# Performance work log

Measured on AMD Instinct MI355X. Metric: run time of the kernel, lower is better.

The kernel has to match this reference:

```python
import jax, jax.numpy as jnp
import numpy as np

D_MODEL = 1024
N_HEADS = 16
HEAD_DIM = D_MODEL // N_HEADS
MAX_REL = 16
SEQ = 1024
BATCH = 4


def _rel_embed(table, length_q, length_k):
    # table: [2*MAX_REL+1, head_dim] -> [lq, lk, head_dim]
    dist = jnp.arange(length_k)[None, :] - jnp.arange(length_q)[:, None]
    idx = jnp.clip(dist, -MAX_REL, MAX_REL) + MAX_REL
    return table[idx]


def setup_inputs() -> dict:
    key = jax.random.key(0)
    ks = jax.random.split(key, 16)
    s = 1.0 / np.sqrt(D_MODEL)
    inp = {
        "query": jax.random.normal(ks[0], (BATCH, SEQ, D_MODEL), jnp.float32),
        "key": jax.random.normal(ks[1], (BATCH, SEQ, D_MODEL), jnp.float32),
        "value": jax.random.normal(ks[2], (BATCH, SEQ, D_MODEL), jnp.float32),
        "mask": jnp.ones((BATCH, SEQ, SEQ), jnp.int32),
        "Wq": jax.random.normal(ks[3], (D_MODEL, D_MODEL), jnp.float32) * s,
        "bq": jnp.zeros((D_MODEL,), jnp.float32),
        "Wk": jax.random.normal(ks[4], (D_MODEL, D_MODEL), jnp.float32) * s,
        "bk": jnp.zeros((D_MODEL,), jnp.float32),
        "Wv": jax.random.normal(ks[5], (D_MODEL, D_MODEL), jnp.float32) * s,
        "bv": jnp.zeros((D_MODEL,), jnp.float32),
        "Wo": jax.random.normal(ks[6], (D_MODEL, D_MODEL), jnp.float32) * s,
        "bo": jnp.zeros((D_MODEL,), jnp.float32),
        "emb_k": jax.random.normal(ks[7], (2 * MAX_REL + 1, HEAD_DIM), jnp.float32) * 0.1,
        "emb_v": jax.random.normal(ks[8], (2 * MAX_REL + 1, HEAD_DIM), jnp.float32) * 0.1,
    }
    return inp


def reference(query, key, value, mask, Wq, bq, Wk, bk, Wv, bv, Wo, bo, emb_k, emb_v):
    B, lq, _ = query.shape
    H, hd = N_HEADS, HEAD_DIM
    scale = jnp.sqrt(jnp.asarray(hd, query.dtype))

    q = (query @ Wq.T + bq).reshape(B, lq, H, hd)   # [B,S,H,hd]
    k = (key @ Wk.T + bk).reshape(B, lq, H, hd)
    v = (value @ Wv.T + bv).reshape(B, lq, H, hd)

    # content-content term
    attn1 = jnp.einsum("bqhd,bkhd->bhqk", q, k)
    # content-position term: r_k2[q,k,d]
    r_k2 = _rel_embed(emb_k, lq, lq)               # [S,S,hd]
    attn2 = jnp.einsum("bqhd,qkd->bhqk", q, r_k2)

    attn = (attn1 + attn2) / scale
    attn = jnp.where(mask[:, None, :, :] == 0, -jnp.inf, attn)
    attn = jax.nn.softmax(attn, axis=-1)           # [B,H,S,S]

    weight1 = jnp.einsum("bhqk,bkhd->bhqd", attn, v)
    r_v2 = _rel_embed(emb_v, lq, lq)               # [S,S,hd]
    weight2 = jnp.einsum("bhqk,qkd->bhqd", attn, r_v2)

    x = (weight1 + weight2).transpose(0, 2, 1, 3).reshape(B, lq, H * hd)
    return x @ Wo.T + bo
```

## Files before the change

### kernel.cpp

```cpp
#include <hip/hip_runtime.h>
#include <math.h>

#define D_MODEL 1024
#define N_HEADS 16
#define HEAD_DIM 64
#define MAX_REL 16
#define SEQ 1024
#define BATCH 4

typedef _Float16 f16x8 __attribute__((ext_vector_type(8)));
typedef _Float16 f16x4 __attribute__((ext_vector_type(4)));
typedef _Float16 f16x2 __attribute__((ext_vector_type(2)));
typedef float f32x4 __attribute__((ext_vector_type(4)));
typedef unsigned long long u64;

__device__ __forceinline__ void gld_lds16(const _Float16* g, _Float16* l) {
    __builtin_amdgcn_global_load_lds(
        (const __attribute__((address_space(1))) void*)(uintptr_t)g,
        (__attribute__((address_space(3))) void*)(uintptr_t)l, 16, 0, 0);
}

__global__ __launch_bounds__(256) void mask_compress(
    const int* __restrict__ mask, u64* __restrict__ mbits, int n64)
{
    const int wid  = (blockIdx.x * 256 + threadIdx.x) >> 6;
    const int lane = threadIdx.x & 63;
    if (wid < n64) {
        const int vv = mask[(size_t)wid * 64 + lane];
        const u64 bal = __ballot(vv != 0);
        if (lane == 0) mbits[wid] = bal;
    }
}

__global__ __launch_bounds__(256) void cvt_all(
    const float* __restrict__ q, const float* __restrict__ k, const float* __restrict__ v,
    const float* __restrict__ Wq, const float* __restrict__ Wk,
    const float* __restrict__ Wv, const float* __restrict__ Wo,
    _Float16* __restrict__ qin, _Float16* __restrict__ kin, _Float16* __restrict__ vin,
    _Float16* __restrict__ wq, _Float16* __restrict__ wk,
    _Float16* __restrict__ wv, _Float16* __restrict__ wo)
{
    const size_t M1 = 1u << 20;
    size_t f = ((size_t)blockIdx.x * 256 + threadIdx.x) * 4;
    const float* src; _Float16* dst; size_t off;
    if (f < 4*M1)       { src = q; dst = qin; off = f; }
    else if (f < 8*M1)  { src = k; dst = kin; off = f - 4*M1; }
    else if (f < 12*M1) { src = v; dst = vin; off = f - 8*M1; }
    else {
        int u = (int)(f >> 20) - 12;
        src = (u==0)?Wq:(u==1)?Wk:(u==2)?Wv:Wo;
        dst = (u==0)?wq:(u==1)?wk:(u==2)?wv:wo;
        off = f & (M1 - 1);
    }
    float4 x = *(const float4*)(src + off);
    f16x4 h; h[0]=(_Float16)x.x; h[1]=(_Float16)x.y; h[2]=(_Float16)x.z; h[3]=(_Float16)x.w;
    *(f16x4*)(dst + off) = h;
}

#define TBM 64
#define TBN 64
#define TBK 64

template <typename CT>
__global__ __launch_bounds__(256, 4) void gemm_f16async(
    const _Float16* A0, const _Float16* A1, const _Float16* A2,
    const _Float16* W0, const _Float16* W1, const _Float16* W2,
    const float* b0, const float* b1, const float* b2,
    CT* C0, CT* C1, CT* C2, int M, int N, int K)
{
    __shared__ _Float16 As[2][TBM * TBK];
    __shared__ _Float16 Ws[2][TBN * TBK];

    const int z = blockIdx.z;
    const _Float16* A = (z==0)?A0:(z==1)?A1:A2;
    const _Float16* W = (z==0)?W0:(z==1)?W1:W2;
    const float* bias = (z==0)?b0:(z==1)?b1:b2;
    CT* C = (z==0)?C0:(z==1)?C1:C2;

    const int tid = threadIdx.x;
    const int lane = tid & 63;
    const int w = tid >> 6;
    const int quad = lane >> 4;
    const int l16 = lane & 15;
    const int m0 = blockIdx.y * TBM;
    const int n0 = blockIdx.x * TBN;
    const int wm = (w & 1) * 32;
    const int wn = (w >> 1) * 32;

    int em[2], ek[2];
    #pragma unroll
    for (int i = 0; i < 2; ++i) {
        const int e = i * 256 + tid;
        em[i] = e >> 3;
        ek[i] = (e & 7) ^ (em[i] & 7);
    }

    f32x4 acc[2][2];
    #pragma unroll
    for (int i = 0; i < 2; ++i)
        #pragma unroll
        for (int j = 0; j < 2; ++j)
            acc[i][j] = (f32x4){0.f, 0.f, 0.f, 0.f};

    const int nk = K / TBK;

    #pragma unroll
    for (int i = 0; i < 2; ++i) {
        const int e = i * 256 + tid;
        gld_lds16(A + (size_t)(m0 + em[i]) * K + ek[i] * 8, &As[0][e * 8]);
        gld_lds16(W + (size_t)(n0 + em[i]) * K + ek[i] * 8, &Ws[0][e * 8]);
    }
    __syncthreads();

    for (int it = 0; it < nk; ++it) {
        const int cur = it & 1, nb = cur ^ 1;

        if (it + 1 < nk) {
            const int kt = (it + 1) * TBK;
            #pragma unroll
            for (int i = 0; i < 2; ++i) {
                const int e = i * 256 + tid;
                gld_lds16(A + (size_t)(m0 + em[i]) * K + kt + ek[i] * 8, &As[nb][e * 8]);
                gld_lds16(W + (size_t)(n0 + em[i]) * K + kt + ek[i] * 8, &Ws[nb][e * 8]);
            }
        }

        #pragma unroll
        for (int ks = 0; ks < 2; ++ks) {
            const int k8 = ks * 4 + quad;
            f16x8 af[2], bf[2];
            #pragma unroll
            for (int i = 0; i < 2; ++i) {
                const int m = wm + i * 16 + l16;
                af[i] = *(const f16x8*)&As[cur][m * 64 + ((k8 ^ (m & 7)) * 8)];
            }
            #pragma unroll
            for (int j = 0; j < 2; ++j) {
                const int n = wn + j * 16 + l16;
                bf[j] = *(const f16x8*)&Ws[cur][n * 64 + ((k8 ^ (n & 7)) * 8)];
            }
            #pragma unroll
            for (int i = 0; i < 2; ++i)
                #pragma unroll
                for (int j = 0; j < 2; ++j)
                    acc[i][j] = __builtin_amdgcn_mfma_f32_16x16x32_f16(af[i], bf[j], acc[i][j], 0, 0, 0);
        }
        __syncthreads();
    }

    const int cbase = n0 + wn + l16;
    const int rbase = m0 + wm + quad * 4;
    #pragma unroll
    for (int j = 0; j < 2; ++j) {
        const int col = cbase + j * 16;
        const float bv = bias[col];
        #pragma unroll
        for (int i = 0; i < 2; ++i) {
            #pragma unroll
            for (int r = 0; r < 4; ++r) {
                const int m = rbase + i * 16 + r;
                C[(size_t)m * N + col] = (CT)(acc[i][j][r] + bv);
            }
        }
    }
}

#define QT 64
#define KT 64
#define SP 72
#define EVW 32
#define NT (SEQ/KT)

__global__ __launch_bounds__(256, 2) void attn_flash_mfma3(
    const _Float16* __restrict__ q, const _Float16* __restrict__ kg,
    const _Float16* __restrict__ v, const u64* __restrict__ mbits,
    const float* __restrict__ emb_k, const float* __restrict__ emb_v,
    _Float16* __restrict__ x)
{
    __shared__ _Float16 Ks[2][KT * HEAD_DIM];
    __shared__ _Float16 Vt[2][HEAD_DIM * SP];
    __shared__ _Float16 Ps[QT * SP];
    __shared__ _Float16 EvT[HEAD_DIM * EVW];
    __shared__ _Float16 pbh[QT * 33];
    __shared__ _Float16 bandh[QT * 33];

    const int qt = blockIdx.x, h = blockIdx.y, b = blockIdx.z;
    const int q0 = qt * QT;
    const int tid = threadIdx.x;
    const int lane = tid & 63;
    const int w = tid >> 6;
    const int quad = lane >> 4;
    const int l16 = lane & 15;
    const int qrow = w * 16 + quad * 4;

    const int vk = (tid & 31) * 2, vd = (tid >> 5) * 8;
    const int k8 = vk >> 3, klo = vk & 7;
    const int sr = tid >> 2, sc = (tid & 3) * 16;

    const float CS = 0.18033688011112042f;
    const float M8 = 8.0f;

    #pragma unroll
    for (int i = 0; i < 2; ++i) {
        const int e = i * 256 + tid;
        const int row = e >> 3;
        const int k8s = (e & 7) ^ (row & 7);
        gld_lds16(kg + ((size_t)(b*SEQ + row))*D_MODEL + h*HEAD_DIM + k8s*8, &Ks[0][e*8]);
    }

    f16x8 qf[2];
    {
        const _Float16* qp = q + ((size_t)(b*SEQ + q0 + w*16 + l16))*D_MODEL + h*HEAD_DIM;
        qf[0] = *(const f16x8*)(qp + quad*8);
        qf[1] = *(const f16x8*)(qp + 32 + quad*8);
    }

    f16x8 vp0, vp1;
    {
        const _Float16* vp = v + ((size_t)(b*SEQ + vk))*D_MODEL + h*HEAD_DIM + vd;
        vp0 = *(const f16x8*)(vp);
        vp1 = *(const f16x8*)(vp + D_MODEL);
    }

    if (sr < 48) {
        #pragma unroll
        for (int c = 0; c < 16; ++c) {
            float val = (sr < 33) ? emb_k[sr*HEAD_DIM + sc + c] : 0.f;
            Ps[sr*SP + sc + c] = (_Float16)val;
        }
    }
    for (int idx = tid; idx < HEAD_DIM*EVW; idx += 256) {
        const int d = idx >> 5, j = idx & 31;
        EvT[d*EVW + j] = (_Float16)emb_v[j*HEAD_DIM + d];
    }
    for (int i = tid; i < QT*33; i += 256) bandh[i] = (_Float16)(-60000.f);
    __syncthreads();

    {
        f32x4 accP[3];
        #pragma unroll
        for (int jt = 0; jt < 3; ++jt) accP[jt] = (f32x4){0.f,0.f,0.f,0.f};
        #pragma unroll
        for (int ks2 = 0; ks2 < 2; ++ks2) {
            const int ko = ks2*32 + quad*8;
            #pragma unroll
            for (int jt = 0; jt < 3; ++jt) {
                f16x8 bf = *(const f16x8*)&Ps[(jt*16 + l16)*SP + ko];
                accP[jt] = __builtin_amdgcn_mfma_f32_16x16x32_f16(qf[ks2], bf, accP[jt], 0, 0, 0);
            }
        }
        #pragma unroll
        for (int jt = 0; jt < 3; ++jt) {
            const int j = jt*16 + l16;
            if (j < 33) {
                #pragma unroll
                for (int r = 0; r < 4; ++r) pbh[(qrow + r)*33 + j] = (_Float16)(accP[jt][r] * CS);
            }
        }
    }
    __syncthreads();

    #pragma unroll
    for (int i = 0; i < 8; ++i) {
        const int d = vd + i;
        const int xd = (d >> 3) & 7;
        f16x2 pr; pr[0] = vp0[i]; pr[1] = vp1[i];
        *(f16x2*)&Vt[0][d*SP + ((k8 ^ xd) << 3) + klo] = pr;
    }
    __syncthreads();

    f32x4 accO[4];
    #pragma unroll
    for (int dt = 0; dt < 4; ++dt) accO[dt] = (f32x4){0.f,0.f,0.f,0.f};
    f32x4 accL = (f32x4){0.f,0.f,0.f,0.f};
    f32x4 accRT = (f32x4){0.f,0.f,0.f,0.f};
    float rt1[4] = {0.f,0.f,0.f,0.f};

    f16x8 ones;
    #pragma unroll
    for (int i = 0; i < 8; ++i) ones[i] = (_Float16)1.0f;

    const int kxl = l16 & 7;

    for (int t = 0; t < NT; ++t) {
        const int cur = t & 1, nb = cur ^ 1;
        const int k0 = t * KT;
        const int kq = k0 - q0;
        const int mode = (kq <= -128) ? 0 : (kq >= 128 ? 2 : 1);

        if (t + 1 < NT) {
            #pragma unroll
            for (int i = 0; i < 2; ++i) {
                const int e = i * 256 + tid;
                const int row = e >> 3;
                const int k8s = (e & 7) ^ (row & 7);
                gld_lds16(kg + ((size_t)(b*SEQ + k0 + KT + row))*D_MODEL + h*HEAD_DIM + k8s*8, &Ks[nb][e*8]);
            }
            const _Float16* vp = v + ((size_t)(b*SEQ + k0 + KT + vk))*D_MODEL + h*HEAD_DIM + vd;
            vp0 = *(const f16x8*)(vp);
            vp1 = *(const f16x8*)(vp + D_MODEL);
        }

        u64 mw[4];
        {
            const u64* mb = mbits + ((size_t)(b*SEQ + q0 + qrow)) * (SEQ/64) + t;
            #pragma unroll
            for (int r = 0; r < 4; ++r) mw[r] = mb[(size_t)r * (SEQ/64)];
        }

        f32x4 accS[4];
        #pragma unroll
        for (int jt = 0; jt < 4; ++jt) accS[jt] = (f32x4){0.f,0.f,0.f,0.f};
        #pragma unroll
        for (int ks2 = 0; ks2 < 2; ++ks2) {
            const int slot = (ks2*4 + quad) ^ kxl;
            #pragma unroll
            for (int jt = 0; jt < 4; ++jt) {
                f16x8 bf = *(const f16x8*)&Ks[cur][(jt*16 + l16)*64 + (slot << 3)];
                accS[jt] = __builtin_amdgcn_mfma_f32_16x16x32_f16(qf[ks2], bf, accS[jt], 0, 0, 0);
            }
        }

        const bool fm = __all((mw[0] & mw[1] & mw[2] & mw[3]) == ~0ull) != 0;

        if (mode != 1) {
            float pc[4];
            const int ii = (mode == 0) ? 0 : 32;
            #pragma unroll
            for (int r = 0; r < 4; ++r) pc[r] = (float)pbh[(qrow + r)*33 + ii] - M8;
            if (fm) {
                #pragma unroll
                for (int jt = 0; jt < 4; ++jt) {
                    const int kl = jt*16 + l16;
                    #pragma unroll
                    for (int r = 0; r < 4; ++r) {
                        const float p = __builtin_amdgcn_exp2f(fmaf(accS[jt][r], CS, pc[r]));
                        Ps[(qrow + r)*SP + kl] = (_Float16)p;
                    }
                }
            } else {
                #pragma unroll
                for (int jt = 0; jt < 4; ++jt) {
                    const int kl = jt*16 + l16;
                    #pragma unroll
                    for (int r = 0; r < 4; ++r) {
                        float s = fmaf(accS[jt][r], CS, pc[r]);
                        if (!((mw[r] >> kl) & 1ull)) s = -1e30f;
                        Ps[(qrow + r)*SP + kl] = (_Float16)__builtin_amdgcn_exp2f(s);
                    }
                }
            }
        } else {
            float rts[4] = {0.f,0.f,0.f,0.f};
            #pragma unroll
            for (int jt = 0; jt < 4; ++jt) {
                const int kl = jt*16 + l16;
                #pragma unroll
                for (int r = 0; r < 4; ++r) {
                    const int dk = (k0 + kl) - (q0 + qrow + r);
                    const int ii = (dk < -MAX_REL ? -MAX_REL : (dk > MAX_REL ? MAX_REL : dk)) + MAX_REL;
                    float s = fmaf(accS[jt][r], CS, (float)pbh[(qrow + r)*33 + ii]) - M8;
                    if (!((mw[r] >> kl) & 1ull)) s = -1e30f;
                    const float p = __builtin_amdgcn_exp2f(s);
                    if (dk > MAX_REL) rts[r] += p;
                    else if (dk >= -MAX_REL) bandh[(qrow + r)*33 + dk + MAX_REL] = (_Float16)s;
                    Ps[(qrow + r)*SP + kl] = (_Float16)p;
                }
            }
            #pragma unroll
            for (int r = 0; r < 4; ++r) {
                #pragma unroll
                for (int d = 1; d < 16; d <<= 1) rts[r] += __shfl_xor(rts[r], d);
                rt1[r] += rts[r];
            }
        }

        #pragma unroll
        for (int ks2 = 0; ks2 < 2; ++ks2) {
            const int ko = ks2*32 + quad*8;
            const int k8n = ks2*4 + quad;
            f16x8 pf = *(const f16x8*)&Ps[(w*16 + l16)*SP + ko];
            accL = __builtin_amdgcn_mfma_f32_16x16x32_f16(pf, ones, accL, 0, 0, 0);
            if (mode == 2)
                accRT = __builtin_amdgcn_mfma_f32_16x16x32_f16(pf, ones, accRT, 0, 0, 0);
            #pragma unroll
            for (int dt = 0; dt < 4; ++dt) {
                const int d = dt*16 + l16;
                const int xd = (d >> 3) & 7;
                f16x8 vf = *(const f16x8*)&Vt[cur][d*SP + ((k8n ^ xd) << 3)];
                accO[dt] = __builtin_amdgcn_mfma_f32_16x16x32_f16(pf, vf, accO[dt], 0, 0, 0);
            }
        }

        if (t + 1 < NT) {
            #pragma unroll
            for (int i = 0; i < 8; ++i) {
                const int d = vd + i;
                const int xd = (d >> 3) & 7;
                f16x2 pr; pr[0] = vp0[i]; pr[1] = vp1[i];
                *(f16x2*)&Vt[nb][d*SP + ((k8 ^ xd) << 3) + klo] = pr;
            }
        }
        __syncthreads();
    }

    float ej0[4], ej1[4], e32[4], bsp[4];
    #pragma unroll
    for (int r = 0; r < 4; ++r) {
        const int ql = qrow + r;
        ej0[r] = __builtin_amdgcn_exp2f((float)bandh[ql*33 + l16]);
        ej1[r] = __builtin_amdgcn_exp2f((float)bandh[ql*33 + 16 + l16]);
        e32[r] = __builtin_amdgcn_exp2f((float)bandh[ql*33 + 32]);
        bsp[r] = ej0[r] + ej1[r];
    }
    #pragma unroll
    for (int r = 0; r < 4; ++r) {
        #pragma unroll
        for (int d = 1; d < 16; d <<= 1) bsp[r] += __shfl_xor(bsp[r], d);
    }
    #pragma unroll
    for (int r = 0; r < 4; ++r) {
        const int ql = qrow + r;
        const float rt = accRT[r] + rt1[r];
        const float Pl = accL[r] - rt - (bsp[r] + e32[r]);
        Ps[ql*SP + l16]      = (_Float16)((l16 == 0) ? (ej0[r] + Pl) : ej0[r]);
        Ps[ql*SP + 16 + l16] = (_Float16)ej1[r];
    }

    f32x4 accW[4];
    #pragma unroll
    for (int dt = 0; dt < 4; ++dt) accW[dt] = (f32x4){0.f,0.f,0.f,0.f};
    {
        f16x8 pf = *(const f16x8*)&Ps[(w*16 + l16)*SP + quad*8];
        #pragma unroll
        for (int dt = 0; dt < 4; ++dt) {
            f16x8 ef = *(const f16x8*)&EvT[(dt*16 + l16)*EVW + quad*8];
            accW[dt] = __builtin_amdgcn_mfma_f32_16x16x32_f16(pf, ef, accW[dt], 0, 0, 0);
        }
    }
    #pragma unroll
    for (int r = 0; r < 4; ++r) {
        const float p32 = e32[r] + accRT[r] + rt1[r];
        const float linv = 1.f / accL[r];
        const int qg = q0 + qrow + r;
        #pragma unroll
        for (int dt = 0; dt < 4; ++dt) {
            const float w32 = emb_v[32*HEAD_DIM + dt*16 + l16];
            x[((size_t)(b*SEQ + qg))*D_MODEL + h*HEAD_DIM + dt*16 + l16] =
                (_Float16)((accO[dt][r] + accW[dt][r] + p32 * w32) * linv);
        }
    }
}

extern "C" void kernel_launch(void* const* d_in, const int* in_sizes, int n_in,
                              void* d_out, int out_size, void* d_ws, size_t ws_size,
                              hipStream_t stream) {
    const float* query = (const float*)d_in[0];
    const float* key   = (const float*)d_in[1];
    const float* value = (const float*)d_in[2];
    const int*   mask  = (const int*)d_in[3];
    const float* Wq = (const float*)d_in[4];
    const float* bq = (const float*)d_in[5];
    const float* Wk = (const float*)d_in[6];
    const float* bk = (const float*)d_in[7];
    const float* Wv = (const float*)d_in[8];
    const float* bv = (const float*)d_in[9];
    const float* Wo = (const float*)d_in[10];
    const float* bo = (const float*)d_in[11];
    const float* emb_k = (const float*)d_in[12];
    const float* emb_v = (const float*)d_in[13];
    float* out = (float*)d_out;

    const size_t M1 = 1u << 20;
    _Float16* ws16 = (_Float16*)d_ws;
    _Float16* qin = ws16;
    _Float16* kin = ws16 + 4*M1;
    _Float16* vin = ws16 + 8*M1;
    _Float16* qp  = ws16 + 12*M1;
    _Float16* kp  = ws16 + 16*M1;
    _Float16* vp  = ws16 + 20*M1;
    _Float16* wq16 = ws16 + 24*M1;
    _Float16* wk16 = ws16 + 25*M1;
    _Float16* wv16 = ws16 + 26*M1;
    _Float16* wo16 = ws16 + 27*M1;
    u64* mbits = (u64*)(ws16 + 28*M1);
    _Float16* xh = qin;

    const int Mrows = BATCH * SEQ;
    const int n64 = BATCH * SEQ * (SEQ / 64);

    cvt_all<<<dim3(16384), dim3(256), 0, stream>>>(
        query, key, value, Wq, Wk, Wv, Wo,
        qin, kin, vin, wq16, wk16, wv16, wo16);

    mask_compress<<<dim3((n64*64)/256), dim3(256), 0, stream>>>(mask, mbits, n64);

    dim3 gQKV(D_MODEL / TBN, Mrows / TBM, 3), tB(256);
    gemm_f16async<_Float16><<<gQKV, tB, 0, stream>>>(
        qin, kin, vin, wq16, wk16, wv16, bq, bk, bv, qp, kp, vp,
        Mrows, D_MODEL, D_MODEL);

    dim3 gA(SEQ/QT, N_HEADS, BATCH);
    attn_flash_mfma3<<<gA, dim3(256), 0, stream>>>(qp, kp, vp, mbits, emb_k, emb_v, xh);

    dim3 gO(D_MODEL / TBN, Mrows / TBM, 1);
    gemm_f16async<float><<<gO, tB, 0, stream>>>(
        xh, xh, xh, wo16, wo16, wo16, bo, bo, bo, out, out, out,
        Mrows, D_MODEL, D_MODEL);
}
```

Baseline: 264.4 us.

## Fuse fp32-to-fp16 conversion into GEMM tile loads, drop separate convert kernel

Removes the standalone cvt_all kernel and has the GEMMs load fp32 inputs and weights directly, converting to fp16 in registers before storing to LDS. The QKV GEMM reads fp32 activations and weights, and the output GEMM reads fp32 Wo. This removes a full extra read/write pass over about 16M elements. The cost is double the global bytes per tile load, register staging in place of async global-to-LDS loads, and each weight tile being re-converted by many blocks. Launch bounds drop to 3 blocks per SM to make room for the staging registers.

```diff
diff --git a/kernel.cpp b/kernel.cpp
--- a/kernel.cpp
+++ b/kernel.cpp
@@ -18,6 +18,15 @@
     __builtin_amdgcn_global_load_lds(
         (const __attribute__((address_space(1))) void*)(uintptr_t)g,
         (__attribute__((address_space(3))) void*)(uintptr_t)l, 16, 0, 0);
+}
+
+__device__ __forceinline__ f16x8 ld_cvt8(const float* p) {
+    float4 lo = *(const float4*)(p);
+    float4 hi = *(const float4*)(p + 4);
+    f16x8 h;
+    h[0]=(_Float16)lo.x; h[1]=(_Float16)lo.y; h[2]=(_Float16)lo.z; h[3]=(_Float16)lo.w;
+    h[4]=(_Float16)hi.x; h[5]=(_Float16)hi.y; h[6]=(_Float16)hi.z; h[7]=(_Float16)hi.w;
+    return h;
 }
 
 __global__ __launch_bounds__(256) void mask_compress(
@@ -32,39 +41,14 @@
     }
 }
 
-__global__ __launch_bounds__(256) void cvt_all(
-    const float* __restrict__ q, const float* __restrict__ k, const float* __restrict__ v,
-    const float* __restrict__ Wq, const float* __restrict__ Wk,
-    const float* __restrict__ Wv, const float* __restrict__ Wo,
-    _Float16* __restrict__ qin, _Float16* __restrict__ kin, _Float16* __restrict__ vin,
-    _Float16* __restrict__ wq, _Float16* __restrict__ wk,
-    _Float16* __restrict__ wv, _Float16* __restrict__ wo)
-{
-    const size_t M1 = 1u << 20;
-    size_t f = ((size_t)blockIdx.x * 256 + threadIdx.x) * 4;
-    const float* src; _Float16* dst; size_t off;
-    if (f < 4*M1)       { src = q; dst = qin; off = f; }
-    else if (f < 8*M1)  { src = k; dst = kin; off = f - 4*M1; }
-    else if (f < 12*M1) { src = v; dst = vin; off = f - 8*M1; }
-    else {
-        int u = (int)(f >> 20) - 12;
-        src = (u==0)?Wq:(u==1)?Wk:(u==2)?Wv:Wo;
-        dst = (u==0)?wq:(u==1)?wk:(u==2)?wv:wo;
-        off = f & (M1 - 1);
-    }
-    float4 x = *(const float4*)(src + off);
-    f16x4 h; h[0]=(_Float16)x.x; h[1]=(_Float16)x.y; h[2]=(_Float16)x.z; h[3]=(_Float16)x.w;
-    *(f16x4*)(dst + off) = h;
-}
-
 #define TBM 64
 #define TBN 64
 #define TBK 64
 
-template <typename CT>
-__global__ __launch_bounds__(256, 4) void gemm_f16async(
-    const _Float16* A0, const _Float16* A1, const _Float16* A2,
-    const _Float16* W0, const _Float16* W1, const _Float16* W2,
+template <typename AT, typename WT, typename CT>
+__global__ __launch_bounds__(256, 3) void gemm_mixed(
+    const AT* A0, const AT* A1, const AT* A2,
+    const WT* W0, const WT* W1, const WT* W2,
     const float* b0, const float* b1, const float* b2,
     CT* C0, CT* C1, CT* C2, int M, int N, int K)
 {
@@ -72,8 +56,8 @@
     __shared__ _Float16 Ws[2][TBN * TBK];
 
     const int z = blockIdx.z;
-    const _Float16* A = (z==0)?A0:(z==1)?A1:A2;
-    const _Float16* W = (z==0)?W0:(z==1)?W1:W2;
+    const AT* A = (z==0)?A0:(z==1)?A1:A2;
+    const WT* W = (z==0)?W0:(z==1)?W1:W2;
     const float* bias = (z==0)?b0:(z==1)?b1:b2;
     CT* C = (z==0)?C0:(z==1)?C1:C2;
 
@@ -107,21 +91,39 @@
     #pragma unroll
     for (int i = 0; i < 2; ++i) {
         const int e = i * 256 + tid;
-        gld_lds16(A + (size_t)(m0 + em[i]) * K + ek[i] * 8, &As[0][e * 8]);
-        gld_lds16(W + (size_t)(n0 + em[i]) * K + ek[i] * 8, &Ws[0][e * 8]);
+        if constexpr (sizeof(AT) == 4) {
+            *(f16x8*)&As[0][e * 8] = ld_cvt8(A + (size_t)(m0 + em[i]) * K + ek[i] * 8);
+        } else {
+            gld_lds16(A + (size_t)(m0 + em[i]) * K + ek[i] * 8, &As[0][e * 8]);
+        }
+        if constexpr (sizeof(WT) == 4) {
+            *(f16x8*)&Ws[0][e * 8] = ld_cvt8(W + (size_t)(n0 + em[i]) * K + ek[i] * 8);
+        } else {
+            gld_lds16(W + (size_t)(n0 + em[i]) * K + ek[i] * 8, &Ws[0][e * 8]);
+        }
     }
     __syncthreads();
 
     for (int it = 0; it < nk; ++it) {
         const int cur = it & 1, nb = cur ^ 1;
-
-        if (it + 1 < nk) {
+        const bool havenext = (it + 1 < nk);
+
+        f16x8 stA[2], stW[2];
+        if (havenext) {
             const int kt = (it + 1) * TBK;
             #pragma unroll
             for (int i = 0; i < 2; ++i) {
                 const int e = i * 256 + tid;
-                gld_lds16(A + (size_t)(m0 + em[i]) * K + kt + ek[i] * 8, &As[nb][e * 8]);
-                gld_lds16(W + (size_t)(n0 + em[i]) * K + kt + ek[i] * 8, &Ws[nb][e * 8]);
+                if constexpr (sizeof(AT) == 4) {
+                    stA[i] = ld_cvt8(A + (size_t)(m0 + em[i]) * K + kt + ek[i] * 8);
+                } else {
+                    gld_lds16(A + (size_t)(m0 + em[i]) * K + kt + ek[i] * 8, &As[nb][e * 8]);
+                }
+                if constexpr (sizeof(WT) == 4) {
+                    stW[i] = ld_cvt8(W + (size_t)(n0 + em[i]) * K + kt + ek[i] * 8);
+                } else {
+                    gld_lds16(W + (size_t)(n0 + em[i]) * K + kt + ek[i] * 8, &Ws[nb][e * 8]);
+                }
             }
         }
 
@@ -144,6 +146,15 @@
                 #pragma unroll
                 for (int j = 0; j < 2; ++j)
                     acc[i][j] = __builtin_amdgcn_mfma_f32_16x16x32_f16(af[i], bf[j], acc[i][j], 0, 0, 0);
+        }
+
+        if (havenext) {
+            #pragma unroll
+            for (int i = 0; i < 2; ++i) {
+                const int e = i * 256 + tid;
+                if constexpr (sizeof(AT) == 4) *(f16x8*)&As[nb][e * 8] = stA[i];
+                if constexpr (sizeof(WT) == 4) *(f16x8*)&Ws[nb][e * 8] = stW[i];
+            }
         }
         __syncthreads();
     }
@@ -473,38 +484,27 @@
 
     const size_t M1 = 1u << 20;
     _Float16* ws16 = (_Float16*)d_ws;
-    _Float16* qin = ws16;
-    _Float16* kin = ws16 + 4*M1;
-    _Float16* vin = ws16 + 8*M1;
-    _Float16* qp  = ws16 + 12*M1;
-    _Float16* kp  = ws16 + 16*M1;
-    _Float16* vp  = ws16 + 20*M1;
-    _Float16* wq16 = ws16 + 24*M1;
-    _Float16* wk16 = ws16 + 25*M1;
-    _Float16* wv16 = ws16 + 26*M1;
-    _Float16* wo16 = ws16 + 27*M1;
-    u64* mbits = (u64*)(ws16 + 28*M1);
-    _Float16* xh = qin;
+    _Float16* qp  = ws16;
+    _Float16* kp  = ws16 + 4*M1;
+    _Float16* vp  = ws16 + 8*M1;
+    _Float16* xh  = ws16 + 12*M1;
+    u64* mbits = (u64*)(ws16 + 16*M1);
 
     const int Mrows = BATCH * SEQ;
     const int n64 = BATCH * SEQ * (SEQ / 64);
 
-    cvt_all<<<dim3(16384), dim3(256), 0, stream>>>(
-        query, key, value, Wq, Wk, Wv, Wo,
-        qin, kin, vin, wq16, wk16, wv16, wo16);
-
     mask_compress<<<dim3((n64*64)/256), dim3(256), 0, stream>>>(mask, mbits, n64);
 
     dim3 gQKV(D_MODEL / TBN, Mrows / TBM, 3), tB(256);
-    gemm_f16async<_Float16><<<gQKV, tB, 0, stream>>>(
-        qin, kin, vin, wq16, wk16, wv16, bq, bk, bv, qp, kp, vp,
+    gemm_mixed<float, float, _Float16><<<gQKV, tB, 0, stream>>>(
+        query, key, value, Wq, Wk, Wv, bq, bk, bv, qp, kp, vp,
         Mrows, D_MODEL, D_MODEL);
 
     dim3 gA(SEQ/QT, N_HEADS, BATCH);
     attn_flash_mfma3<<<gA, dim3(256), 0, stream>>>(qp, kp, vp, mbits, emb_k, emb_v, xh);
 
     dim3 gO(D_MODEL / TBN, Mrows / TBM, 1);
-    gemm_f16async<float><<<gO, tB, 0, stream>>>(
-        xh, xh, xh, wo16, wo16, wo16, bo, bo, bo, out, out, out,
+    gemm_mixed<_Float16, float, float><<<gO, tB, 0, stream>>>(
+        xh, xh, xh, Wo, Wo, Wo, bo, bo, bo, out, out, out,
         Mrows, D_MODEL, D_MODEL);
 }
```

New measurement: 296.9 us. 1.12x slower.
